# Kernel tuning notes

Hardware: AMD Instinct MI355X
Metric: run time of the kernel (lower is better)

The kernel has to match this reference:

```python
import jax, jax.numpy as jnp
import numpy as np

ALPHA, BETA, THRESH, T = 0.9, 0.8, 1.0, 10


def _heaviside(x):
    return (x > 0).astype(x.dtype)


def _conv(x, w, b, stride):
    y = jax.lax.conv_general_dilated(
        x, w, window_strides=(stride, stride), padding='VALID',
        dimension_numbers=('NCHW', 'OIHW', 'NCHW'))
    return jax.nn.relu(y + b[None, :, None, None])


def setup_inputs() -> dict:
    key = jax.random.key(0)
    ks = jax.random.split(key, 16)
    B = 128
    state = jax.random.uniform(ks[0], (B, 3, 224, 224), dtype=jnp.float32)
    history = jax.random.uniform(ks[1], (B, 90), dtype=jnp.float32)
    fc_in = 64 * 24 * 24 + 90  # 36954

    def w(k, shape, fan_in):
        return jax.random.normal(k, shape, dtype=jnp.float32) * (1.0 / np.sqrt(fan_in))

    return {
        'state': state, 'history': history,
        'cw1': w(ks[2], (32, 3, 8, 8), 3 * 8 * 8), 'cb1': jnp.zeros((32,), jnp.float32),
        'cw2': w(ks[3], (64, 32, 4, 4), 32 * 4 * 4), 'cb2': jnp.zeros((64,), jnp.float32),
        'cw3': w(ks[4], (64, 64, 3, 3), 64 * 3 * 3), 'cb3': jnp.zeros((64,), jnp.float32),
        'w1': w(ks[5], (128, fc_in), fc_in), 'b1': jnp.zeros((128,), jnp.float32),
        'w2': w(ks[6], (256, 128), 128), 'b2': jnp.zeros((256,), jnp.float32),
        'w3': w(ks[7], (9, 256), 256), 'b3': jnp.zeros((9,), jnp.float32),
    }


def reference(state, history, cw1, cb1, cw2, cb2, cw3, cb3, w1, b1, w2, b2, w3, b3):
    B = state.shape[0]
    f = _conv(state, cw1, cb1, 4)
    f = _conv(f, cw2, cb2, 2)
    f = _conv(f, cw3, cb3, 1)
    x = jnp.concatenate([f.reshape(B, -1), history], axis=1)  # (B, 36954)
    # encoding='constant' -> input (hence h1) is identical every timestep
    h1 = x @ w1.T + b1  # (B,128)

    def lif(h, mem, syn):
        new_syn = ALPHA * syn + h
        new_mem = BETA * mem + new_syn
        out = _heaviside(new_mem - THRESH)
        return out, new_mem - out * THRESH, new_syn

    z = lambda d: jnp.zeros((B, d), x.dtype)
    carry0 = (z(128), z(128), z(256), z(256), z(9), z(9), z(9))

    def step(carry, _):
        mem1, syn1, mem2, syn2, mem3, syn3, pot = carry
        spk1, mem1, syn1 = lif(h1, mem1, syn1)
        h2 = spk1 @ w2.T + b2
        spk2, mem2, syn2 = lif(h2, mem2, syn2)
        h3 = spk2 @ w3.T + b3
        syn3 = ALPHA * syn3 + h3
        mem3 = BETA * mem3 + syn3
        pot = pot + mem3
        return (mem1, syn1, mem2, syn2, mem3, syn3, pot), None

    carry, _ = jax.lax.scan(step, carry0, None, length=T)
    return carry[6] / T
```

## Files before the change

### kernel.cpp

```cpp
#include <hip/hip_runtime.h>

#define ALPHA 0.9f
#define BETA  0.8f
#define XS 36960

typedef _Float16 f16;
typedef _Float16 f16x8 __attribute__((ext_vector_type(8)));
typedef float f32x4 __attribute__((ext_vector_type(4)));


__global__ __launch_bounds__(256) void prep_weights_kernel(
    const float* __restrict__ cw1, const float* __restrict__ cw2,
    const float* __restrict__ cw3, const float* __restrict__ w2,
    f16* __restrict__ w1h, f16* __restrict__ w1l,
    f16* __restrict__ w2h, f16* __restrict__ w2l,
    f16* __restrict__ w3h, f16* __restrict__ w3l,
    float* __restrict__ w2q) {
  int i = blockIdx.x * 256 + threadIdx.x;
  if (i < 6144)  { float v = cw1[i]; f16 h = (f16)v; w1h[i] = h; w1l[i] = (f16)(v - (float)h); }
  if (i < 32768) { float v = cw2[i]; f16 h = (f16)v; w2h[i] = h; w2l[i] = (f16)(v - (float)h); }
  if (i < 49152) {
    int oc = i / 768, r = i % 768;
    int c = r / 12, rr = r % 12, kh = rr >> 2, kw = rr & 3;
    float v = (kw < 3) ? cw3[oc * 576 + c * 9 + kh * 3 + kw] : 0.f;
    f16 h = (f16)v; w3h[i] = h; w3l[i] = (f16)(v - (float)h);
  }
  if (i < 32768) {
    int j = i >> 7, k = i & 127;
    w2q[((k >> 2) * 256 + j) * 4 + (k & 3)] = w2[i];
  }
}

__global__ __launch_bounds__(256) void pad_w1_kernel(
    const float* __restrict__ w1, float* __restrict__ w1p) {
  int i = blockIdx.x * 256 + threadIdx.x;
  if (i < 128 * 18480) {
    int j = i / 18480, c = i - j * 18480;
    float2 v;
    if (c < 18477) v = *(const float2*)&w1[(size_t)j * 36954 + c * 2];
    else v = make_float2(0.f, 0.f);
    *(float2*)&w1p[(size_t)j * XS + c * 2] = v;
  }
}

template<int IC, int KH, int KWP, int KWV, int S, int IH, int IW,
         int OW, int OHW, int OC, int NPB, bool OUT_X>
__global__ __launch_bounds__(256) void mfma_conv_kernel(
    const float* __restrict__ in, const f16* __restrict__ wh,
    const f16* __restrict__ wl, const float* __restrict__ bias,
    float* __restrict__ out) {
  constexpr int K = IC * KH * KWP;
  constexpr int KCH = K / 32;
  constexpr int MTILES = OC / 16;
  constexpr int NTILES = NPB / 16;
  constexpr int WOC = MTILES / 2;
  constexpr int ASLOTS = OC * 4;
  constexpr int BSLOTS = NPB * 4;
  constexpr int SITER = BSLOTS / 256;
  __shared__ f16 Ah[MTILES * 512], Al[MTILES * 512];
  __shared__ f16 Bh[NTILES * 512], Bl[NTILES * 512];

  const int n = blockIdx.y;
  const int pos0 = blockIdx.x * NPB;
  const int t = threadIdx.x;
  const int w = t >> 6, lane = t & 63, quad = lane >> 4, l16 = lane & 15;
  const int woc  = (WOC == 1) ? 0 : (w & 1);
  const int wpos = (WOC == 1) ? w : (w >> 1);
  const size_t in_n = (size_t)n * IC * IH * IW;

  int ohS[SITER], owS[SITER], kq8[SITER];
#pragma unroll
  for (int si = 0; si < SITER; ++si) {
    int s = t + si * 256;
    int nt = s >> 6, prem = s & 15;
    int pos = pos0 + nt * 16 + prem;
    if (pos > OHW - 1) pos = OHW - 1;
    int oh = pos / OW, ow = pos - oh * OW;
    ohS[si] = oh * S; owS[si] = ow * S;
    kq8[si] = ((s >> 4) & 3) * 8;
  }
  const int am = (t >> 6) * 16 + (t & 15);
  const int ak = ((t >> 4) & 3) * 8;

  f32x4 acc[2][2] = {};

  for (int kt = 0; kt < KCH; ++kt) {
    __syncthreads();
    if (t < ASLOTS) {
      *(f16x8*)&Ah[t * 8] = *(const f16x8*)&wh[am * K + kt * 32 + ak];
      *(f16x8*)&Al[t * 8] = *(const f16x8*)&wl[am * K + kt * 32 + ak];
    }
#pragma unroll
    for (int si = 0; si < SITER; ++si) {
      int s = t + si * 256;
      int kb = kt * 32 + kq8[si];
      f16x8 bh, bl;
#pragma unroll
      for (int half = 0; half < 2; ++half) {
        int kk = kb + half * 4;
        int kw0 = kk & (KWP - 1);
        int row = kk / KWP;
        int c = row / KH, kh = row - c * KH;
        const float* p = in + in_n +
            ((size_t)c * IH + ohS[si] + kh) * IW + owS[si] + kw0;
#pragma unroll
        for (int e = 0; e < 4; ++e) {
          float v = (KWV < KWP && e >= KWV) ? 0.f : p[e];
          f16 h = (f16)v;
          bh[half * 4 + e] = h;
          bl[half * 4 + e] = (f16)(v - (float)h);
        }
      }
      *(f16x8*)&Bh[s * 8] = bh;
      *(f16x8*)&Bl[s * 8] = bl;
    }
    __syncthreads();
    f16x8 ah0 = *(const f16x8*)&Ah[(woc * 2 + 0) * 512 + lane * 8];
    f16x8 ah1 = *(const f16x8*)&Ah[(woc * 2 + 1) * 512 + lane * 8];
    f16x8 al0 = *(const f16x8*)&Al[(woc * 2 + 0) * 512 + lane * 8];
    f16x8 al1 = *(const f16x8*)&Al[(woc * 2 + 1) * 512 + lane * 8];
    f16x8 bh0 = *(const f16x8*)&Bh[(wpos * 2 + 0) * 512 + lane * 8];
    f16x8 bh1 = *(const f16x8*)&Bh[(wpos * 2 + 1) * 512 + lane * 8];
    f16x8 bl0 = *(const f16x8*)&Bl[(wpos * 2 + 0) * 512 + lane * 8];
    f16x8 bl1 = *(const f16x8*)&Bl[(wpos * 2 + 1) * 512 + lane * 8];
    acc[0][0] = __builtin_amdgcn_mfma_f32_16x16x32_f16(ah0, bh0, acc[0][0], 0, 0, 0);
    acc[0][0] = __builtin_amdgcn_mfma_f32_16x16x32_f16(ah0, bl0, acc[0][0], 0, 0, 0);
    acc[0][0] = __builtin_amdgcn_mfma_f32_16x16x32_f16(al0, bh0, acc[0][0], 0, 0, 0);
    acc[1][0] = __builtin_amdgcn_mfma_f32_16x16x32_f16(ah1, bh0, acc[1][0], 0, 0, 0);
    acc[1][0] = __builtin_amdgcn_mfma_f32_16x16x32_f16(ah1, bl0, acc[1][0], 0, 0, 0);
    acc[1][0] = __builtin_amdgcn_mfma_f32_16x16x32_f16(al1, bh0, acc[1][0], 0, 0, 0);
    acc[0][1] = __builtin_amdgcn_mfma_f32_16x16x32_f16(ah0, bh1, acc[0][1], 0, 0, 0);
    acc[0][1] = __builtin_amdgcn_mfma_f32_16x16x32_f16(ah0, bl1, acc[0][1], 0, 0, 0);
    acc[0][1] = __builtin_amdgcn_mfma_f32_16x16x32_f16(al0, bh1, acc[0][1], 0, 0, 0);
    acc[1][1] = __builtin_amdgcn_mfma_f32_16x16x32_f16(ah1, bh1, acc[1][1], 0, 0, 0);
    acc[1][1] = __builtin_amdgcn_mfma_f32_16x16x32_f16(ah1, bl1, acc[1][1], 0, 0, 0);
    acc[1][1] = __builtin_amdgcn_mfma_f32_16x16x32_f16(al1, bh1, acc[1][1], 0, 0, 0);
  }
#pragma unroll
  for (int mtl = 0; mtl < 2; ++mtl)
#pragma unroll
    for (int ntl = 0; ntl < 2; ++ntl)
#pragma unroll
      for (int r = 0; r < 4; ++r) {
        int oc  = (woc * 2 + mtl) * 16 + quad * 4 + r;
        int pos = pos0 + (wpos * 2 + ntl) * 16 + l16;
        if (pos < OHW) {
          float v = acc[mtl][ntl][r] + bias[oc];
          v = v > 0.f ? v : 0.f;
          if (OUT_X)
            out[(size_t)n * XS + oc * OHW + pos] = v;
          else
            out[((size_t)n * OC + oc) * OHW + pos] = v;
        }
      }
}

__global__ __launch_bounds__(256) void histpack_kernel(
    const float* __restrict__ h, float* __restrict__ x) {
  int i = blockIdx.x * 256 + threadIdx.x;
  if (i < 128 * 96) {
    int n = i / 96, k = i % 96;
    x[(size_t)n * XS + 36864 + k] = (k < 90) ? h[n * 90 + k] : 0.f;
  }
}

#define FC1_KT 289
__global__ __launch_bounds__(256) void fc1_kernel(
    const float* __restrict__ x, const float* __restrict__ w1p,
    float* __restrict__ P) {
  int kt = blockIdx.x;
  int t  = threadIdx.x;
  int bq = t & 15, jq = t >> 4;
  __shared__ float xs[128 * 36];
  __shared__ float wsm[128 * 36];
  float acc[8][8];
#pragma unroll
  for (int bb = 0; bb < 8; ++bb)
#pragma unroll
    for (int jj = 0; jj < 8; ++jj) acc[bb][jj] = 0.f;

  int cs = t & 7;
  int rs = t >> 3;
#pragma unroll 1
  for (int s = 0; s < 4; ++s) {
    int k0 = kt * 128 + s * 32;
    __syncthreads();
#pragma unroll
    for (int p = 0; p < 4; ++p) {
      int r = rs + p * 32;
      int gk = k0 + cs * 4;
      float4 xv, wv;
      if (gk < 36954) {
        xv = *(const float4*)&x[(size_t)r * XS + gk];
        wv = *(const float4*)&w1p[(size_t)r * XS + gk];
      } else {
        xv = make_float4(0.f, 0.f, 0.f, 0.f);
        wv = make_float4(0.f, 0.f, 0.f, 0.f);
      }
      *(float4*)&xs[r * 36 + cs * 4] = xv;
      *(float4*)&wsm[r * 36 + cs * 4] = wv;
    }
    __syncthreads();
#pragma unroll 1
    for (int kk = 0; kk < 32; kk += 4) {
      float4 xv[8], wv[8];
#pragma unroll
      for (int i = 0; i < 8; ++i)
        xv[i] = *(const float4*)&xs[(bq + 16 * i) * 36 + kk];
#pragma unroll
      for (int i = 0; i < 8; ++i)
        wv[i] = *(const float4*)&wsm[(jq + 16 * i) * 36 + kk];
#pragma unroll
      for (int bb = 0; bb < 8; ++bb)
#pragma unroll
        for (int jj = 0; jj < 8; ++jj) {
          acc[bb][jj] = fmaf(xv[bb].x, wv[jj].x, acc[bb][jj]);
          acc[bb][jj] = fmaf(xv[bb].y, wv[jj].y, acc[bb][jj]);
          acc[bb][jj] = fmaf(xv[bb].z, wv[jj].z, acc[bb][jj]);
          acc[bb][jj] = fmaf(xv[bb].w, wv[jj].w, acc[bb][jj]);
        }
    }
  }
  float* Pb = P + (size_t)kt * 16384;
#pragma unroll
  for (int bb = 0; bb < 8; ++bb)
#pragma unroll
    for (int jj = 0; jj < 8; ++jj)
      Pb[(bq + 16 * bb) * 128 + jq + 16 * jj] = acc[bb][jj];
}

__global__ __launch_bounds__(256) void reduce_p_kernel(
    const float* __restrict__ P, const float* __restrict__ b1,
    float* __restrict__ h1s) {
  int idx = blockIdx.x * 256 + threadIdx.x;
  int j = idx & 127;
  float a0 = 0.f, a1 = 0.f, a2 = 0.f, a3 = 0.f;
  int kt = 0;
#pragma unroll 2
  for (; kt + 3 < FC1_KT; kt += 4) {
    a0 += P[(size_t)(kt + 0) * 16384 + idx];
    a1 += P[(size_t)(kt + 1) * 16384 + idx];
    a2 += P[(size_t)(kt + 2) * 16384 + idx];
    a3 += P[(size_t)(kt + 3) * 16384 + idx];
  }
  for (; kt < FC1_KT; ++kt) a0 += P[(size_t)kt * 16384 + idx];
  h1s[idx] = ((a0 + a1) + (a2 + a3)) + b1[j];
}

__global__ __launch_bounds__(256, 1) void recur_kernel(
    const float* __restrict__ h1s,
    const float4* __restrict__ w2q,
    const float* __restrict__ b2,
    const float* __restrict__ w3,
    const float* __restrict__ b3,
    float* __restrict__ out) {
  int b = blockIdx.x;
  int t = threadIdx.x;
  __shared__ float spk1s[128];
  __shared__ float spk2s[256];
  __shared__ float w3s[9 * 256];
  __shared__ float part[9][16];
  float4 w2c[32];
#pragma unroll
  for (int k4 = 0; k4 < 32; ++k4) w2c[k4] = w2q[k4 * 256 + t];
  for (int i = t; i < 9 * 256; i += 256) w3s[i] = w3[i];
  float h1 = (t < 128) ? h1s[b * 128 + t] : 0.f;
  float mem1 = 0.f, syn1 = 0.f, mem2 = 0.f, syn2 = 0.f;
  float b2v = b2[t];
  float mem3 = 0.f, syn3 = 0.f, pot = 0.f;
  float b3v = (t < 9) ? b3[t] : 0.f;
  int j3 = t >> 4, p = t & 15;
  __syncthreads();

  for (int step = 0; step < 10; ++step) {
    if (t < 128) {
      syn1 = ALPHA * syn1 + h1;
      mem1 = BETA * mem1 + syn1;
      float s = (mem1 > 1.0f) ? 1.0f : 0.0f;
      mem1 -= s;
      spk1s[t] = s;
    }
    __syncthreads();
    float h2 = b2v;
#pragma unroll
    for (int k4 = 0; k4 < 32; ++k4) {
      float4 s = *(const float4*)&spk1s[k4 * 4];
      h2 = fmaf(s.x, w2c[k4].x, h2);
      h2 = fmaf(s.y, w2c[k4].y, h2);
      h2 = fmaf(s.z, w2c[k4].z, h2);
      h2 = fmaf(s.w, w2c[k4].w, h2);
    }
    syn2 = ALPHA * syn2 + h2;
    mem2 = BETA * mem2 + syn2;
    float s2 = (mem2 > 1.0f) ? 1.0f : 0.0f;
    mem2 -= s2;
    spk2s[t] = s2;
    __syncthreads();
    if (t < 144) {
      float a = 0.f;
      const float* wr = &w3s[j3 * 256 + p * 16];
      const float* sp = &spk2s[p * 16];
#pragma unroll
      for (int e = 0; e < 16; ++e) a = fmaf(sp[e], wr[e], a);
      part[j3][p] = a;
    }
    __syncthreads();
    if (t < 9) {
      float a = b3v;
#pragma unroll
      for (int p2 = 0; p2 < 16; ++p2) a += part[t][p2];
      syn3 = ALPHA * syn3 + a;
      mem3 = BETA * mem3 + syn3;
      pot += mem3;
    }
  }
  if (t < 9) out[b * 9 + t] = pot * 0.1f;
}

extern "C" void kernel_launch(void* const* d_in, const int* in_sizes, int n_in,
                              void* d_out, int out_size, void* d_ws, size_t ws_size,
                              hipStream_t stream) {
  const float* state   = (const float*)d_in[0];
  const float* history = (const float*)d_in[1];
  const float* cw1 = (const float*)d_in[2];
  const float* cb1 = (const float*)d_in[3];
  const float* cw2 = (const float*)d_in[4];
  const float* cb2 = (const float*)d_in[5];
  const float* cw3 = (const float*)d_in[6];
  const float* cb3 = (const float*)d_in[7];
  const float* w1  = (const float*)d_in[8];
  const float* b1  = (const float*)d_in[9];
  const float* w2  = (const float*)d_in[10];
  const float* b2  = (const float*)d_in[11];
  const float* w3  = (const float*)d_in[12];
  const float* b3  = (const float*)d_in[13];
  float* out = (float*)d_out;
  char* ws = (char*)d_ws;

  float* f1  = (float*)(ws + 0);
  float* xb  = (float*)(ws + 0);
  float* w1p = (float*)(ws + 18923520);
  float* f2  = (float*)(ws + 49561600);
  float* P   = (float*)(ws + 49561600);
  f16* wf1h = (f16*)(ws + 71712768);
  f16* wf1l = (f16*)(ws + 71725056);
  f16* wf2h = (f16*)(ws + 71737344);
  f16* wf2l = (f16*)(ws + 71802880);
  f16* wf3h = (f16*)(ws + 71868416);
  f16* wf3l = (f16*)(ws + 71966720);
  float* w2q = (float*)(ws + 72065024);
  float* h1s = (float*)(ws + 72196096);

  prep_weights_kernel<<<192, 256, 0, stream>>>(cw1, cw2, cw3, w2,
                                               wf1h, wf1l, wf2h, wf2l,
                                               wf3h, wf3l, w2q);
  mfma_conv_kernel<3, 8, 8, 8, 4, 224, 224, 55, 3025, 32, 128, false>
      <<<dim3(24, 128), 256, 0, stream>>>(state, wf1h, wf1l, cb1, f1);
  mfma_conv_kernel<32, 4, 4, 4, 2, 55, 55, 26, 676, 64, 64, false>
      <<<dim3(11, 128), 256, 0, stream>>>(f1, wf2h, wf2l, cb2, f2);
  pad_w1_kernel<<<9240, 256, 0, stream>>>(w1, w1p);
  mfma_conv_kernel<64, 3, 4, 3, 1, 26, 26, 24, 576, 64, 64, true>
      <<<dim3(9, 128), 256, 0, stream>>>(f2, wf3h, wf3l, cb3, xb);
  histpack_kernel<<<48, 256, 0, stream>>>(history, xb);
  fc1_kernel<<<FC1_KT, 256, 0, stream>>>(xb, w1p, P);
  reduce_p_kernel<<<64, 256, 0, stream>>>(P, b1, h1s);
  recur_kernel<<<128, 256, 0, stream>>>(h1s, (const float4*)w2q, b2, w3, b3, out);
}
```

Before: 346.9 us.

## Load conv MFMA operands directly into registers with double-buffered prefetch

```diff
diff --git a/kernel.cpp b/kernel.cpp
--- a/kernel.cpp
+++ b/kernel.cpp
@@ -7,6 +7,8 @@
 typedef _Float16 f16;
 typedef _Float16 f16x8 __attribute__((ext_vector_type(8)));
 typedef float f32x4 __attribute__((ext_vector_type(4)));
+
+struct F4 { float x, y, z, w; };
 
 
 __global__ __launch_bounds__(256) void prep_weights_kernel(
@@ -45,20 +47,16 @@
 
 template<int IC, int KH, int KWP, int KWV, int S, int IH, int IW,
          int OW, int OHW, int OC, int NPB, bool OUT_X>
-__global__ __launch_bounds__(256) void mfma_conv_kernel(
+__global__ __launch_bounds__(256) void direct_conv_kernel(
     const float* __restrict__ in, const f16* __restrict__ wh,
     const f16* __restrict__ wl, const float* __restrict__ bias,
     float* __restrict__ out) {
   constexpr int K = IC * KH * KWP;
   constexpr int KCH = K / 32;
   constexpr int MTILES = OC / 16;
-  constexpr int NTILES = NPB / 16;
   constexpr int WOC = MTILES / 2;
-  constexpr int ASLOTS = OC * 4;
-  constexpr int BSLOTS = NPB * 4;
-  constexpr int SITER = BSLOTS / 256;
-  __shared__ f16 Ah[MTILES * 512], Al[MTILES * 512];
-  __shared__ f16 Bh[NTILES * 512], Bl[NTILES * 512];
+  constexpr bool AL16 = (IW % 4 == 0) && (S % 4 == 0);
+  constexpr int EM = (KWP == 4) ? 3 : 7;
 
   const int n = blockIdx.y;
   const int pos0 = blockIdx.x * NPB;
@@ -66,76 +64,90 @@
   const int w = t >> 6, lane = t & 63, quad = lane >> 4, l16 = lane & 15;
   const int woc  = (WOC == 1) ? 0 : (w & 1);
   const int wpos = (WOC == 1) ? w : (w >> 1);
-  const size_t in_n = (size_t)n * IC * IH * IW;
-
-  int ohS[SITER], owS[SITER], kq8[SITER];
-#pragma unroll
-  for (int si = 0; si < SITER; ++si) {
-    int s = t + si * 256;
-    int nt = s >> 6, prem = s & 15;
-    int pos = pos0 + nt * 16 + prem;
+  const float* __restrict__ inb = in + (size_t)n * IC * IH * IW;
+
+  int posv[2], ohS[2], owS[2];
+#pragma unroll
+  for (int ntl = 0; ntl < 2; ++ntl) {
+    int pos = pos0 + (wpos * 2 + ntl) * 16 + l16;
+    posv[ntl] = pos;
     if (pos > OHW - 1) pos = OHW - 1;
     int oh = pos / OW, ow = pos - oh * OW;
-    ohS[si] = oh * S; owS[si] = ow * S;
-    kq8[si] = ((s >> 4) & 3) * 8;
-  }
-  const int am = (t >> 6) * 16 + (t & 15);
-  const int ak = ((t >> 4) & 3) * 8;
+    ohS[ntl] = oh * S; owS[ntl] = ow * S;
+  }
+  const f16* __restrict__ whp0 = wh + (size_t)((woc * 2 + 0) * 16 + l16) * K;
+  const f16* __restrict__ whp1 = wh + (size_t)((woc * 2 + 1) * 16 + l16) * K;
+  const f16* __restrict__ wlp0 = wl + (size_t)((woc * 2 + 0) * 16 + l16) * K;
+  const f16* __restrict__ wlp1 = wl + (size_t)((woc * 2 + 1) * 16 + l16) * K;
 
   f32x4 acc[2][2] = {};
 
-  for (int kt = 0; kt < KCH; ++kt) {
-    __syncthreads();
-    if (t < ASLOTS) {
-      *(f16x8*)&Ah[t * 8] = *(const f16x8*)&wh[am * K + kt * 32 + ak];
-      *(f16x8*)&Al[t * 8] = *(const f16x8*)&wl[am * K + kt * 32 + ak];
-    }
-#pragma unroll
-    for (int si = 0; si < SITER; ++si) {
-      int s = t + si * 256;
-      int kb = kt * 32 + kq8[si];
-      f16x8 bh, bl;
+  f16x8 rah0[2], rah1[2], ral0[2], ral1[2];
+  float rb[2][2][8];
+
+  auto LOAD = [&](int kt, int buf) {
+    rah0[buf] = *(const f16x8*)&whp0[kt * 32 + quad * 8];
+    rah1[buf] = *(const f16x8*)&whp1[kt * 32 + quad * 8];
+    ral0[buf] = *(const f16x8*)&wlp0[kt * 32 + quad * 8];
+    ral1[buf] = *(const f16x8*)&wlp1[kt * 32 + quad * 8];
+#pragma unroll
+    for (int ntl = 0; ntl < 2; ++ntl)
 #pragma unroll
       for (int half = 0; half < 2; ++half) {
-        int kk = kb + half * 4;
-        int kw0 = kk & (KWP - 1);
-        int row = kk / KWP;
+        int kk = kt * 32 + quad * 8 + half * 4;
+        int row = kk / KWP, kw0 = kk % KWP;
         int c = row / KH, kh = row - c * KH;
-        const float* p = in + in_n +
-            ((size_t)c * IH + ohS[si] + kh) * IW + owS[si] + kw0;
-#pragma unroll
-        for (int e = 0; e < 4; ++e) {
-          float v = (KWV < KWP && e >= KWV) ? 0.f : p[e];
-          f16 h = (f16)v;
-          bh[half * 4 + e] = h;
-          bl[half * 4 + e] = (f16)(v - (float)h);
+        const float* p = inb + ((size_t)c * IH + ohS[ntl] + kh) * IW
+                             + owS[ntl] + kw0;
+        if constexpr (AL16) {
+          float4 v = *(const float4*)p;
+          rb[buf][ntl][half * 4 + 0] = v.x;
+          rb[buf][ntl][half * 4 + 1] = v.y;
+          rb[buf][ntl][half * 4 + 2] = v.z;
+          rb[buf][ntl][half * 4 + 3] = v.w;
+        } else {
+          F4 v = *(const F4*)p;
+          rb[buf][ntl][half * 4 + 0] = v.x;
+          rb[buf][ntl][half * 4 + 1] = v.y;
+          rb[buf][ntl][half * 4 + 2] = v.z;
+          rb[buf][ntl][half * 4 + 3] = v.w;
         }
       }
-      *(f16x8*)&Bh[s * 8] = bh;
-      *(f16x8*)&Bl[s * 8] = bl;
-    }
-    __syncthreads();
-    f16x8 ah0 = *(const f16x8*)&Ah[(woc * 2 + 0) * 512 + lane * 8];
-    f16x8 ah1 = *(const f16x8*)&Ah[(woc * 2 + 1) * 512 + lane * 8];
-    f16x8 al0 = *(const f16x8*)&Al[(woc * 2 + 0) * 512 + lane * 8];
-    f16x8 al1 = *(const f16x8*)&Al[(woc * 2 + 1) * 512 + lane * 8];
-    f16x8 bh0 = *(const f16x8*)&Bh[(wpos * 2 + 0) * 512 + lane * 8];
-    f16x8 bh1 = *(const f16x8*)&Bh[(wpos * 2 + 1) * 512 + lane * 8];
-    f16x8 bl0 = *(const f16x8*)&Bl[(wpos * 2 + 0) * 512 + lane * 8];
-    f16x8 bl1 = *(const f16x8*)&Bl[(wpos * 2 + 1) * 512 + lane * 8];
-    acc[0][0] = __builtin_amdgcn_mfma_f32_16x16x32_f16(ah0, bh0, acc[0][0], 0, 0, 0);
-    acc[0][0] = __builtin_amdgcn_mfma_f32_16x16x32_f16(ah0, bl0, acc[0][0], 0, 0, 0);
-    acc[0][0] = __builtin_amdgcn_mfma_f32_16x16x32_f16(al0, bh0, acc[0][0], 0, 0, 0);
-    acc[1][0] = __builtin_amdgcn_mfma_f32_16x16x32_f16(ah1, bh0, acc[1][0], 0, 0, 0);
-    acc[1][0] = __builtin_amdgcn_mfma_f32_16x16x32_f16(ah1, bl0, acc[1][0], 0, 0, 0);
-    acc[1][0] = __builtin_amdgcn_mfma_f32_16x16x32_f16(al1, bh0, acc[1][0], 0, 0, 0);
-    acc[0][1] = __builtin_amdgcn_mfma_f32_16x16x32_f16(ah0, bh1, acc[0][1], 0, 0, 0);
-    acc[0][1] = __builtin_amdgcn_mfma_f32_16x16x32_f16(ah0, bl1, acc[0][1], 0, 0, 0);
-    acc[0][1] = __builtin_amdgcn_mfma_f32_16x16x32_f16(al0, bh1, acc[0][1], 0, 0, 0);
-    acc[1][1] = __builtin_amdgcn_mfma_f32_16x16x32_f16(ah1, bh1, acc[1][1], 0, 0, 0);
-    acc[1][1] = __builtin_amdgcn_mfma_f32_16x16x32_f16(ah1, bl1, acc[1][1], 0, 0, 0);
-    acc[1][1] = __builtin_amdgcn_mfma_f32_16x16x32_f16(al1, bh1, acc[1][1], 0, 0, 0);
-  }
+  };
+
+  auto COMPUTE = [&](int buf) {
+    f16x8 bh0, bl0, bh1, bl1;
+#pragma unroll
+    for (int e = 0; e < 8; ++e) {
+      float v0 = ((e & EM) >= KWV) ? 0.f : rb[buf][0][e];
+      f16 h0 = (f16)v0;
+      bh0[e] = h0; bl0[e] = (f16)(v0 - (float)h0);
+      float v1 = ((e & EM) >= KWV) ? 0.f : rb[buf][1][e];
+      f16 h1 = (f16)v1;
+      bh1[e] = h1; bl1[e] = (f16)(v1 - (float)h1);
+    }
+    acc[0][0] = __builtin_amdgcn_mfma_f32_16x16x32_f16(rah0[buf], bh0, acc[0][0], 0, 0, 0);
+    acc[0][0] = __builtin_amdgcn_mfma_f32_16x16x32_f16(rah0[buf], bl0, acc[0][0], 0, 0, 0);
+    acc[0][0] = __builtin_amdgcn_mfma_f32_16x16x32_f16(ral0[buf], bh0, acc[0][0], 0, 0, 0);
+    acc[1][0] = __builtin_amdgcn_mfma_f32_16x16x32_f16(rah1[buf], bh0, acc[1][0], 0, 0, 0);
+    acc[1][0] = __builtin_amdgcn_mfma_f32_16x16x32_f16(rah1[buf], bl0, acc[1][0], 0, 0, 0);
+    acc[1][0] = __builtin_amdgcn_mfma_f32_16x16x32_f16(ral1[buf], bh0, acc[1][0], 0, 0, 0);
+    acc[0][1] = __builtin_amdgcn_mfma_f32_16x16x32_f16(rah0[buf], bh1, acc[0][1], 0, 0, 0);
+    acc[0][1] = __builtin_amdgcn_mfma_f32_16x16x32_f16(rah0[buf], bl1, acc[0][1], 0, 0, 0);
+    acc[0][1] = __builtin_amdgcn_mfma_f32_16x16x32_f16(ral0[buf], bh1, acc[0][1], 0, 0, 0);
+    acc[1][1] = __builtin_amdgcn_mfma_f32_16x16x32_f16(rah1[buf], bh1, acc[1][1], 0, 0, 0);
+    acc[1][1] = __builtin_amdgcn_mfma_f32_16x16x32_f16(rah1[buf], bl1, acc[1][1], 0, 0, 0);
+    acc[1][1] = __builtin_amdgcn_mfma_f32_16x16x32_f16(ral1[buf], bh1, acc[1][1], 0, 0, 0);
+  };
+
+  LOAD(0, 0);
+#pragma unroll
+  for (int kt = 0; kt < KCH - 1; ++kt) {
+    LOAD(kt + 1, (kt + 1) & 1);
+    COMPUTE(kt & 1);
+  }
+  COMPUTE((KCH - 1) & 1);
+
 #pragma unroll
   for (int mtl = 0; mtl < 2; ++mtl)
 #pragma unroll
@@ -143,7 +155,7 @@
 #pragma unroll
       for (int r = 0; r < 4; ++r) {
         int oc  = (woc * 2 + mtl) * 16 + quad * 4 + r;
-        int pos = pos0 + (wpos * 2 + ntl) * 16 + l16;
+        int pos = posv[ntl];
         if (pos < OHW) {
           float v = acc[mtl][ntl][r] + bias[oc];
           v = v > 0.f ? v : 0.f;
@@ -354,12 +366,12 @@
   prep_weights_kernel<<<192, 256, 0, stream>>>(cw1, cw2, cw3, w2,
                                                wf1h, wf1l, wf2h, wf2l,
                                                wf3h, wf3l, w2q);
-  mfma_conv_kernel<3, 8, 8, 8, 4, 224, 224, 55, 3025, 32, 128, false>
+  direct_conv_kernel<3, 8, 8, 8, 4, 224, 224, 55, 3025, 32, 128, false>
       <<<dim3(24, 128), 256, 0, stream>>>(state, wf1h, wf1l, cb1, f1);
-  mfma_conv_kernel<32, 4, 4, 4, 2, 55, 55, 26, 676, 64, 64, false>
+  direct_conv_kernel<32, 4, 4, 4, 2, 55, 55, 26, 676, 64, 64, false>
       <<<dim3(11, 128), 256, 0, stream>>>(f1, wf2h, wf2l, cb2, f2);
   pad_w1_kernel<<<9240, 256, 0, stream>>>(w1, w1p);
-  mfma_conv_kernel<64, 3, 4, 3, 1, 26, 26, 24, 576, 64, 64, true>
+  direct_conv_kernel<64, 3, 4, 3, 1, 26, 26, 24, 576, 64, 64, true>
       <<<dim3(9, 128), 256, 0, stream>>>(f2, wf3h, wf3l, cb3, xb);
   histpack_kernel<<<48, 256, 0, stream>>>(history, xb);
   fc1_kernel<<<FC1_KT, 256, 0, stream>>>(xb, w1p, P);
```

New measurement: 419.9 us. 1.21x slower.
